# Kernel tuning notes

Hardware: AMD Instinct MI355X
Metric: run time of the kernel (lower is better)

The kernel has to match this reference:

```python
import jax, jax.numpy as jnp
import numpy as np

B, T, D, U = 16, 1600, 512, 1024


def setup_inputs() -> dict:
    key = jax.random.key(0)
    ks = jax.random.split(key, 7)
    sk = 1.0 / np.sqrt(D)
    sr = 1.0 / np.sqrt(U)
    return {
        "x": jax.random.normal(ks[0], (B, T, D), jnp.float32),
        "x_len": jnp.full((B,), T, dtype=jnp.int32),
        "kernel_f": jax.random.normal(ks[1], (D, 4 * U), jnp.float32) * sk,
        "rkernel_f": jax.random.normal(ks[2], (U, 4 * U), jnp.float32) * sr,
        "bias_f": jnp.zeros((4 * U,), jnp.float32),
        "kernel_b": jax.random.normal(ks[3], (D, 4 * U), jnp.float32) * sk,
        "rkernel_b": jax.random.normal(ks[4], (U, 4 * U), jnp.float32) * sr,
        "bias_b": jnp.zeros((4 * U,), jnp.float32),
    }


def _lstm(x, kernel, rkernel, bias):
    """Keras-semantics LSTM, return_sequences=True. x: [B,T,D] -> [B,T,U]."""
    units = rkernel.shape[0]
    # precompute input projection for all timesteps (the big GEMM)
    xg = jnp.einsum('btd,dg->btg', x, kernel) + bias  # [B,T,4U]
    xg = jnp.swapaxes(xg, 0, 1)  # [T,B,4U] for scan
    h0 = jnp.zeros((x.shape[0], units), x.dtype)
    c0 = jnp.zeros((x.shape[0], units), x.dtype)

    def step(carry, g_in):
        h, c = carry
        g = g_in + h @ rkernel  # [B,4U]
        i, f, cc, o = jnp.split(g, 4, axis=-1)  # Keras gate order i,f,c,o
        c = jax.nn.sigmoid(f) * c + jax.nn.sigmoid(i) * jnp.tanh(cc)
        h = jax.nn.sigmoid(o) * jnp.tanh(c)
        return (h, c), h

    _, hs = jax.lax.scan(step, (h0, c0), xg)  # hs: [T,B,U]
    return jnp.swapaxes(hs, 0, 1)


def reference(x, x_len, kernel_f, rkernel_f, bias_f, kernel_b, rkernel_b, bias_b):
    # Bidirectional(LSTM(units, return_sequences=True)), merge_mode='concat'
    out_f = _lstm(x, kernel_f, rkernel_f, bias_f)
    out_b = _lstm(x[:, ::-1], kernel_b, rkernel_b, bias_b)[:, ::-1]
    outputs = jnp.concatenate([out_f, out_b], axis=-1)  # [B,T,2U]
    return outputs, x_len
```

## Files before the change

### kernel.cpp

```cpp
#include <hip/hip_runtime.h>

#define B_   16
#define T_   1600
#define D_   512
#define U_   1024
#define G_   4096
#define NWG  256
#define TPB  256
#define KTOT 1536
#define APAD 1544
#define ROWB (APAD*2)
#define X16OFF (1 << 18)

typedef __attribute__((ext_vector_type(8))) __bf16 bf16x8;
typedef __attribute__((ext_vector_type(4))) float  f32x4;
typedef __attribute__((ext_vector_type(2))) float  f32x2;
typedef __attribute__((ext_vector_type(4))) unsigned int uint4v;
typedef __attribute__((ext_vector_type(8))) unsigned short us8v;
typedef unsigned long long u64;
typedef unsigned int u32;

__device__ __forceinline__ unsigned short f2bf(float f) {
  unsigned u = __builtin_bit_cast(unsigned, f);
  u += 0x7FFFu + ((u >> 16) & 1u);
  return (unsigned short)(u >> 16);
}
__device__ __forceinline__ bf16x8 cvt8(const float4 a, const float4 b) {
  us8v r;
  r[0]=f2bf(a.x); r[1]=f2bf(a.y); r[2]=f2bf(a.z); r[3]=f2bf(a.w);
  r[4]=f2bf(b.x); r[5]=f2bf(b.y); r[6]=f2bf(b.z); r[7]=f2bf(b.w);
  return __builtin_bit_cast(bf16x8, r);
}
__device__ __forceinline__ float sigm(float x){ return 1.f / (1.f + __expf(-x)); }
__device__ __forceinline__ float tanh_(float x){ return 1.f - 2.f / (__expf(2.f*x) + 1.f); }

extern "C" __global__ void __launch_bounds__(256)
xcvt_kernel(const float* __restrict__ xin, unsigned short* __restrict__ x16) {
  const size_t i = ((size_t)blockIdx.x*256 + threadIdx.x) * 8;
  float4 a = *(const float4*)(xin + i);
  float4 b = *(const float4*)(xin + i + 4);
  *(us8v*)(x16 + i) = __builtin_bit_cast(us8v, cvt8(a, b));
}

extern "C" __global__ void __launch_bounds__(TPB, 1)
bilstm_kernel(const float* __restrict__ x, const int* __restrict__ xlen,
              const float* __restrict__ kf, const float* __restrict__ rkf, const float* __restrict__ bf_,
              const float* __restrict__ kb, const float* __restrict__ rkb, const float* __restrict__ bb_,
              float* __restrict__ out, u32* __restrict__ hbuf32,
              const unsigned short* __restrict__ x16, int use16)
{
  extern __shared__ char smem[];

  const int tid = threadIdx.x;
  const int wg  = blockIdx.x;
  const int dir = wg >> 7;
  const int slot = wg & 127;
  const int u0  = slot << 3;

  if (wg == 0 && tid < B_)
    out[(size_t)B_*T_*2*U_ + tid] = (float)xlen[tid];

  const float* Km = dir ? kb  : kf;
  const float* Rm = dir ? rkb : rkf;
  const float* Bv = dir ? bb_ : bf_;

  const int w = tid >> 6, l = tid & 63;
  const int ntile = w & 1, khalf = w >> 1;

  {
    char* Wb = smem;
    for (int i = tid; i < KTOT*32; i += TPB) {
      int k = i >> 5, c = i & 31;
      int gc = ((c >> 3) << 10) + u0 + (c & 7);
      float wv = (k < D_) ? Km[(size_t)k*G_ + gc] : Rm[(size_t)(k-D_)*G_ + gc];
      *(unsigned short*)(Wb + c*ROWB + (k << 1)) = f2bf(wv);
    }
  }
  __syncthreads();

  bf16x8 wx[8], wh[16];
  {
    const char* Brow = smem + (ntile*16 + (l & 15))*ROWB + ((l >> 4) << 4);
    #pragma unroll
    for (int i = 0; i < 8; ++i)  wx[i] = *(const bf16x8*)(Brow + ((khalf*8 + i) << 6));
    #pragma unroll
    for (int i = 0; i < 16; ++i) wh[i] = *(const bf16x8*)(Brow + ((16 + khalf*16 + i) << 6));
  }
  __syncthreads();

  float* gates = (float*)smem;
  char*  hst   = smem + 4096;
  float* gp    = gates + khalf*512;
  const int drow0 = (l >> 4) << 2, dcol = ntile*16 + (l & 15);

  const int eb = tid >> 2, eup = (tid & 3) << 1;
  float bi0=0, bi1=0, bff0=0, bff1=0, bz0=0, bz1=0, bo0=0, bo1=0, c0=0, c1=0;
  if (tid < 64) {
    bi0 = Bv[u0+eup];        bi1 = Bv[u0+eup+1];
    bff0= Bv[1024+u0+eup];   bff1= Bv[1024+u0+eup+1];
    bz0 = Bv[2048+u0+eup];   bz1 = Bv[2048+u0+eup+1];
    bo0 = Bv[3072+u0+eup];   bo1 = Bv[3072+u0+eup+1];
  }

  const float* xbase = x + (size_t)(l & 15)*T_*D_ + khalf*256 + ((l >> 4) << 3);
  const unsigned short* x16b = x16 + (size_t)(l & 15)*T_*D_ + khalf*256 + ((l >> 4) << 3);

  const char* hrow  = hst + (l & 15)*2048;
  const int   kbase = (khalf*512 + ((l >> 4) << 3)) << 1;
  const int   swz   = ((l & 15) & 7) << 4;

  const unsigned off0 = (unsigned)tid * 16;

  f32x4 acc = {0.f, 0.f, 0.f, 0.f};
  {
    const int tg0 = dir ? (T_ - 1) : 0;
    if (use16) {
      const unsigned short* xA = x16b + (size_t)tg0 * D_;
      #pragma unroll
      for (int i = 0; i < 8; ++i)
        acc = __builtin_amdgcn_mfma_f32_16x16x32_bf16(*(const bf16x8*)(xA + i*32), wx[i], acc, 0, 0, 0);
    } else {
      const float* xA = xbase + (size_t)tg0 * D_;
      #pragma unroll
      for (int i = 0; i < 8; ++i) {
        float4 lo = *(const float4*)(xA + i*32);
        float4 hi = *(const float4*)(xA + i*32 + 4);
        acc = __builtin_amdgcn_mfma_f32_16x16x32_bf16(cvt8(lo, hi), wx[i], acc, 0, 0, 0);
      }
    }
  }

  for (int t = 0; t < T_; ++t) {
    const int tg = dir ? (T_ - 1 - t) : t;

    if (t > 0) {
      const u32* hb = hbuf32 + (size_t)((t & 1)*2 + dir) * 16384;
      const unsigned tagv = (unsigned)t << 16;
      uint4v hv[16];
      long long guard = 0;
      for (;;) {
        #pragma unroll
        for (int j = 0; j < 16; ++j)
          asm volatile("global_load_dwordx4 %0, %1, %2 sc0 sc1"
                       : "=v"(hv[j]) : "v"(off0 + (unsigned)(j*4096)), "s"(hb));
        asm volatile("s_waitcnt vmcnt(0)" ::: "memory");
        __builtin_amdgcn_sched_barrier(0);
        unsigned bad = 0;
        #pragma unroll
        for (int j = 0; j < 16; ++j)
          bad |= (hv[j][0] ^ tagv) | (hv[j][2] ^ tagv);
        if (!(bad & 0xFFFF0000u)) break;
        __builtin_amdgcn_s_sleep(1);
        if (++guard > (1LL << 22)) break;
      }
      #pragma unroll
      for (int j = 0; j < 16; ++j) {
        u32 lo = __builtin_amdgcn_perm(hv[j][1], hv[j][0], 0x05040100u);
        u32 hi = __builtin_amdgcn_perm(hv[j][3], hv[j][2], 0x05040100u);
        u64 v = ((u64)hi << 32) | lo;
        *(u64*)(hst + j*2048 + ((tid << 3) ^ ((j & 7) << 4))) = v;
      }
      __syncthreads();

      f32x4 acc2 = {0.f, 0.f, 0.f, 0.f};
      #pragma unroll
      for (int i = 0; i < 16; i += 2) {
        bf16x8 a0 = *(const bf16x8*)(hrow + ((kbase + i*64)     ^ swz));
        bf16x8 a1 = *(const bf16x8*)(hrow + ((kbase + (i+1)*64) ^ swz));
        acc  = __builtin_amdgcn_mfma_f32_16x16x32_bf16(a0, wh[i],   acc,  0, 0, 0);
        acc2 = __builtin_amdgcn_mfma_f32_16x16x32_bf16(a1, wh[i+1], acc2, 0, 0, 0);
      }
      acc[0]+=acc2[0]; acc[1]+=acc2[1]; acc[2]+=acc2[2]; acc[3]+=acc2[3];
    }

    #pragma unroll
    for (int j = 0; j < 4; ++j) gp[(drow0 + j)*32 + dcol] = acc[j];
    __syncthreads();

    if (tid < 64) {
      const float* g0 = gates + eb*32 + eup;
      float gi0 = g0[0]  + g0[512] + bi0,  gi1 = g0[1]  + g0[513] + bi1;
      float gf0 = g0[8]  + g0[520] + bff0, gf1 = g0[9]  + g0[521] + bff1;
      float gz0 = g0[16] + g0[528] + bz0,  gz1 = g0[17] + g0[529] + bz1;
      float go0 = g0[24] + g0[536] + bo0,  go1 = g0[25] + g0[537] + bo1;
      c0 = sigm(gf0)*c0 + sigm(gi0)*tanh_(gz0);
      c1 = sigm(gf1)*c1 + sigm(gi1)*tanh_(gz1);
      float h0 = sigm(go0)*tanh_(c0);
      float h1 = sigm(go1)*tanh_(c1);
      const unsigned tagw = (unsigned)(t + 1) << 16;
      u32 w0 = (u32)f2bf(h0) | tagw;
      u32 w1 = (u32)f2bf(h1) | tagw;
      u32* hdst = hbuf32 + (size_t)(((t & 1) ^ 1)*2 + dir)*16384 + (eb << 10) + u0 + eup;
      __hip_atomic_store((u64*)hdst, ((u64)w1 << 32) | w0, __ATOMIC_RELAXED, __HIP_MEMORY_SCOPE_AGENT);
      f32x2 ho; ho.x = h0; ho.y = h1;
      *(f32x2*)(out + ((size_t)eb*T_ + tg)*(2*U_) + (dir << 10) + u0 + eup) = ho;
    }

    if (t + 1 < T_) {
      const int tg1 = dir ? (T_ - 2 - t) : (t + 1);
      f32x4 nacc = {0.f, 0.f, 0.f, 0.f};
      if (use16) {
        const unsigned short* xA = x16b + (size_t)tg1 * D_;
        #pragma unroll
        for (int i = 0; i < 8; ++i)
          nacc = __builtin_amdgcn_mfma_f32_16x16x32_bf16(*(const bf16x8*)(xA + i*32), wx[i], nacc, 0, 0, 0);
      } else {
        const float* xA = xbase + (size_t)tg1 * D_;
        #pragma unroll
        for (int i = 0; i < 8; ++i) {
          float4 lo = *(const float4*)(xA + i*32);
          float4 hi = *(const float4*)(xA + i*32 + 4);
          nacc = __builtin_amdgcn_mfma_f32_16x16x32_bf16(cvt8(lo, hi), wx[i], nacc, 0, 0, 0);
        }
      }
      acc = nacc;
    }
  }
}

extern "C" void kernel_launch(void* const* d_in, const int* in_sizes, int n_in,
                              void* d_out, int out_size, void* d_ws, size_t ws_size,
                              hipStream_t stream) {
  const float* x   = (const float*)d_in[0];
  const int*   xl  = (const int*)d_in[1];
  const float* kf  = (const float*)d_in[2];
  const float* rkf = (const float*)d_in[3];
  const float* bf_ = (const float*)d_in[4];
  const float* kb  = (const float*)d_in[5];
  const float* rkb = (const float*)d_in[6];
  const float* bb_ = (const float*)d_in[7];
  float* out = (float*)d_out;

  u32* hbuf32 = (u32*)d_ws;
  unsigned short* x16 = (unsigned short*)((char*)d_ws + X16OFF);

  const size_t need = (size_t)X16OFF + (size_t)B_*T_*D_*2;
  const int use16 = (ws_size >= need) ? 1 : 0;

  (void)hipMemsetAsync(d_ws, 0, X16OFF, stream);
  if (use16)
    xcvt_kernel<<<6400, 256, 0, stream>>>(x, x16);

  const size_t smem = 32*(size_t)ROWB;
  bilstm_kernel<<<NWG, TPB, smem, stream>>>(x, xl, kf, rkf, bf_, kb, rkb, bb_,
                                            out, hbuf32, x16, use16);
}
```

Before: 5.185 ms.

## Repartition persistent BiLSTM into 64 large workgroups with LDS-staged x tiles

Shrinks the persistent kernel from 256 workgroups of 256 threads to 64 workgroups of 1024 threads, each owning 32 units (128 gate columns) instead of 8. Fewer workgroups take part in the per-step cross-workgroup spin on the tagged h buffer, and each thread polls 4 loads instead of 16. The x tile is now staged cooperatively into LDS and consumed by MFMA after the barrier, replacing per-wave prefetch from global memory. The trade-off is more work and LDS traffic per workgroup on each serial timestep, and only 64 CUs in use.

```diff
diff --git a/kernel.cpp b/kernel.cpp
--- a/kernel.cpp
+++ b/kernel.cpp
@@ -5,11 +5,14 @@
 #define D_   512
 #define U_   1024
 #define G_   4096
-#define NWG  256
-#define TPB  256
-#define KTOT 1536
-#define APAD 1544
-#define ROWB (APAD*2)
+#define NWG  64
+#define TPB  1024
+#define NCOL 128
+#define GSTR 132
+#define SSTR 392
+#define XBOFF 16896
+#define HOFF  33280
+#define SMEM_BYTES 100352
 #define X16OFF (1 << 18)
 
 typedef __attribute__((ext_vector_type(8))) __bf16 bf16x8;
@@ -51,11 +54,11 @@
 {
   extern __shared__ char smem[];
 
-  const int tid = threadIdx.x;
-  const int wg  = blockIdx.x;
-  const int dir = wg >> 7;
-  const int slot = wg & 127;
-  const int u0  = slot << 3;
+  const int tid  = threadIdx.x;
+  const int wg   = blockIdx.x;
+  const int dir  = wg >> 5;
+  const int slot = wg & 31;
+  const int u0   = slot << 5;
 
   if (wg == 0 && tid < B_)
     out[(size_t)B_*T_*2*U_ + tid] = (float)xlen[tid];
@@ -65,68 +68,76 @@
   const float* Bv = dir ? bb_ : bf_;
 
   const int w = tid >> 6, l = tid & 63;
-  const int ntile = w & 1, khalf = w >> 1;
-
-  {
-    char* Wb = smem;
-    for (int i = tid; i < KTOT*32; i += TPB) {
-      int k = i >> 5, c = i & 31;
-      int gc = ((c >> 3) << 10) + u0 + (c & 7);
-      float wv = (k < D_) ? Km[(size_t)k*G_ + gc] : Rm[(size_t)(k-D_)*G_ + gc];
-      *(unsigned short*)(Wb + c*ROWB + (k << 1)) = f2bf(wv);
-    }
-  }
-  __syncthreads();
+  const int ntile = w >> 1, khalf = w & 1;
+  const int fr8 = (l >> 4) << 3;
+  const int col = ntile*16 + (l & 15);
 
   bf16x8 wx[8], wh[16];
   {
-    const char* Brow = smem + (ntile*16 + (l & 15))*ROWB + ((l >> 4) << 4);
+    unsigned short* stag = (unsigned short*)smem;
     #pragma unroll
-    for (int i = 0; i < 8; ++i)  wx[i] = *(const bf16x8*)(Brow + ((khalf*8 + i) << 6));
+    for (int p = 0; p < 4; ++p) {
+      for (int i = tid; i < 384*NCOL; i += TPB) {
+        int kl = i >> 7, c = i & 127;
+        int k = p*384 + kl;
+        int gc = (c >> 5)*1024 + u0 + (c & 31);
+        float wv = (k < D_) ? Km[(size_t)k*G_ + gc] : Rm[(size_t)(k-D_)*G_ + gc];
+        stag[c*SSTR + kl] = f2bf(wv);
+      }
+      __syncthreads();
+      const unsigned short* srow = stag + col*SSTR;
+      #pragma unroll
+      for (int i = 0; i < 8; ++i) {
+        int kb_ = khalf*256 + i*32;
+        if (kb_/384 == p) wx[i] = *(const bf16x8*)(srow + (kb_ - p*384) + fr8);
+      }
+      #pragma unroll
+      for (int i = 0; i < 16; ++i) {
+        int kb_ = 512 + khalf*512 + i*32;
+        if (kb_/384 == p) wh[i] = *(const bf16x8*)(srow + (kb_ - p*384) + fr8);
+      }
+      __syncthreads();
+    }
+  }
+
+  float* gates = (float*)smem;
+  char*  xbuf  = smem + XBOFF;
+  char*  hst   = smem + HOFF;
+  float* gp    = gates + khalf*(16*GSTR);
+  const int drow0 = (l >> 4) << 2;
+
+  const int eb = tid >> 4, eu = (tid & 15) << 1;
+  float bias[8]; float cc0 = 0.f, cc1 = 0.f;
+  if (tid < 256) {
     #pragma unroll
-    for (int i = 0; i < 16; ++i) wh[i] = *(const bf16x8*)(Brow + ((16 + khalf*16 + i) << 6));
-  }
-  __syncthreads();
-
-  float* gates = (float*)smem;
-  char*  hst   = smem + 4096;
-  float* gp    = gates + khalf*512;
-  const int drow0 = (l >> 4) << 2, dcol = ntile*16 + (l & 15);
-
-  const int eb = tid >> 2, eup = (tid & 3) << 1;
-  float bi0=0, bi1=0, bff0=0, bff1=0, bz0=0, bz1=0, bo0=0, bo1=0, c0=0, c1=0;
-  if (tid < 64) {
-    bi0 = Bv[u0+eup];        bi1 = Bv[u0+eup+1];
-    bff0= Bv[1024+u0+eup];   bff1= Bv[1024+u0+eup+1];
-    bz0 = Bv[2048+u0+eup];   bz1 = Bv[2048+u0+eup+1];
-    bo0 = Bv[3072+u0+eup];   bo1 = Bv[3072+u0+eup+1];
-  }
-
-  const float* xbase = x + (size_t)(l & 15)*T_*D_ + khalf*256 + ((l >> 4) << 3);
-  const unsigned short* x16b = x16 + (size_t)(l & 15)*T_*D_ + khalf*256 + ((l >> 4) << 3);
-
-  const char* hrow  = hst + (l & 15)*2048;
-  const int   kbase = (khalf*512 + ((l >> 4) << 3)) << 1;
-  const int   swz   = ((l & 15) & 7) << 4;
+    for (int g = 0; g < 4; ++g) {
+      bias[g]     = Bv[g*1024 + u0 + eu];
+      bias[4 + g] = Bv[g*1024 + u0 + eu + 1];
+    }
+  }
+
+  const int sxb = tid >> 6, sxk = (tid & 63) << 3;
+  const unsigned short* x16row = x16 + (size_t)sxb*T_*D_ + sxk;
+  const float*          xf32row = x + (size_t)sxb*T_*D_ + sxk;
+  char* xdst = xbuf + sxb*1024;
+  const int xswz = (sxb & 7) << 4;
+
+  const char* xrow = xbuf + (l & 15)*1024;
+  const char* hrow = hst + (l & 15)*2048;
+  const int   swz  = ((l & 15) & 7) << 4;
 
   const unsigned off0 = (unsigned)tid * 16;
-
-  f32x4 acc = {0.f, 0.f, 0.f, 0.f};
+  const int hb_b0 = tid >> 8;
+  const int hb_u  = (tid & 255) << 2;
+
   {
     const int tg0 = dir ? (T_ - 1) : 0;
     if (use16) {
-      const unsigned short* xA = x16b + (size_t)tg0 * D_;
-      #pragma unroll
-      for (int i = 0; i < 8; ++i)
-        acc = __builtin_amdgcn_mfma_f32_16x16x32_bf16(*(const bf16x8*)(xA + i*32), wx[i], acc, 0, 0, 0);
+      *(bf16x8*)(xdst + ((sxk << 1) ^ xswz)) = *(const bf16x8*)(x16row + (size_t)tg0*D_);
     } else {
-      const float* xA = xbase + (size_t)tg0 * D_;
-      #pragma unroll
-      for (int i = 0; i < 8; ++i) {
-        float4 lo = *(const float4*)(xA + i*32);
-        float4 hi = *(const float4*)(xA + i*32 + 4);
-        acc = __builtin_amdgcn_mfma_f32_16x16x32_bf16(cvt8(lo, hi), wx[i], acc, 0, 0, 0);
-      }
+      float4 a = *(const float4*)(xf32row + (size_t)tg0*D_);
+      float4 b = *(const float4*)(xf32row + (size_t)tg0*D_ + 4);
+      *(bf16x8*)(xdst + ((sxk << 1) ^ xswz)) = cvt8(a, b);
     }
   }
 
@@ -136,84 +147,90 @@
     if (t > 0) {
       const u32* hb = hbuf32 + (size_t)((t & 1)*2 + dir) * 16384;
       const unsigned tagv = (unsigned)t << 16;
-      uint4v hv[16];
+      uint4v hv[4];
       long long guard = 0;
       for (;;) {
         #pragma unroll
-        for (int j = 0; j < 16; ++j)
+        for (int j = 0; j < 4; ++j)
           asm volatile("global_load_dwordx4 %0, %1, %2 sc0 sc1"
-                       : "=v"(hv[j]) : "v"(off0 + (unsigned)(j*4096)), "s"(hb));
+                       : "=v"(hv[j]) : "v"(off0 + (unsigned)(j*16384)), "s"(hb));
         asm volatile("s_waitcnt vmcnt(0)" ::: "memory");
         __builtin_amdgcn_sched_barrier(0);
         unsigned bad = 0;
         #pragma unroll
-        for (int j = 0; j < 16; ++j)
+        for (int j = 0; j < 4; ++j)
           bad |= (hv[j][0] ^ tagv) | (hv[j][2] ^ tagv);
         if (!(bad & 0xFFFF0000u)) break;
         __builtin_amdgcn_s_sleep(1);
         if (++guard > (1LL << 22)) break;
       }
       #pragma unroll
-      for (int j = 0; j < 16; ++j) {
+      for (int j = 0; j < 4; ++j) {
         u32 lo = __builtin_amdgcn_perm(hv[j][1], hv[j][0], 0x05040100u);
         u32 hi = __builtin_amdgcn_perm(hv[j][3], hv[j][2], 0x05040100u);
-        u64 v = ((u64)hi << 32) | lo;
-        *(u64*)(hst + j*2048 + ((tid << 3) ^ ((j & 7) << 4))) = v;
-      }
-      __syncthreads();
-
-      f32x4 acc2 = {0.f, 0.f, 0.f, 0.f};
-      #pragma unroll
-      for (int i = 0; i < 16; i += 2) {
-        bf16x8 a0 = *(const bf16x8*)(hrow + ((kbase + i*64)     ^ swz));
-        bf16x8 a1 = *(const bf16x8*)(hrow + ((kbase + (i+1)*64) ^ swz));
-        acc  = __builtin_amdgcn_mfma_f32_16x16x32_bf16(a0, wh[i],   acc,  0, 0, 0);
-        acc2 = __builtin_amdgcn_mfma_f32_16x16x32_bf16(a1, wh[i+1], acc2, 0, 0, 0);
-      }
-      acc[0]+=acc2[0]; acc[1]+=acc2[1]; acc[2]+=acc2[2]; acc[3]+=acc2[3];
-    }
-
-    #pragma unroll
-    for (int j = 0; j < 4; ++j) gp[(drow0 + j)*32 + dcol] = acc[j];
+        const int b = hb_b0 + 4*j;
+        *(u64*)(hst + b*2048 + ((hb_u << 1) ^ ((b & 7) << 4))) = ((u64)hi << 32) | lo;
+      }
+    }
     __syncthreads();
 
-    if (tid < 64) {
-      const float* g0 = gates + eb*32 + eup;
-      float gi0 = g0[0]  + g0[512] + bi0,  gi1 = g0[1]  + g0[513] + bi1;
-      float gf0 = g0[8]  + g0[520] + bff0, gf1 = g0[9]  + g0[521] + bff1;
-      float gz0 = g0[16] + g0[528] + bz0,  gz1 = g0[17] + g0[529] + bz1;
-      float go0 = g0[24] + g0[536] + bo0,  go1 = g0[25] + g0[537] + bo1;
-      c0 = sigm(gf0)*c0 + sigm(gi0)*tanh_(gz0);
-      c1 = sigm(gf1)*c1 + sigm(gi1)*tanh_(gz1);
-      float h0 = sigm(go0)*tanh_(c0);
-      float h1 = sigm(go1)*tanh_(c1);
+    {
+      f32x4 acc = {0.f,0.f,0.f,0.f}, acc2 = acc;
+      #pragma unroll
+      for (int i = 0; i < 8; i += 2) {
+        bf16x8 a0 = *(const bf16x8*)(xrow + (((khalf*8 + i)*64     + (fr8 << 1)) ^ swz));
+        bf16x8 a1 = *(const bf16x8*)(xrow + (((khalf*8 + i + 1)*64 + (fr8 << 1)) ^ swz));
+        acc  = __builtin_amdgcn_mfma_f32_16x16x32_bf16(a0, wx[i],   acc,  0, 0, 0);
+        acc2 = __builtin_amdgcn_mfma_f32_16x16x32_bf16(a1, wx[i+1], acc2, 0, 0, 0);
+      }
+      if (t > 0) {
+        #pragma unroll
+        for (int i = 0; i < 16; i += 2) {
+          bf16x8 a0 = *(const bf16x8*)(hrow + ((khalf*1024 + i*64     + (fr8 << 1)) ^ swz));
+          bf16x8 a1 = *(const bf16x8*)(hrow + ((khalf*1024 + (i+1)*64 + (fr8 << 1)) ^ swz));
+          acc  = __builtin_amdgcn_mfma_f32_16x16x32_bf16(a0, wh[i],   acc,  0, 0, 0);
+          acc2 = __builtin_amdgcn_mfma_f32_16x16x32_bf16(a1, wh[i+1], acc2, 0, 0, 0);
+        }
+      }
+      acc += acc2;
+      #pragma unroll
+      for (int j = 0; j < 4; ++j) gp[(drow0 + j)*GSTR + col] = acc[j];
+    }
+    __syncthreads();
+
+    if (tid < 256) {
+      const float* ga = gates + eb*GSTR + eu;
+      const float* gb2 = gates + (16 + eb)*GSTR + eu;
+      f32x2 ia = *(const f32x2*)(ga);      f32x2 ib = *(const f32x2*)(gb2);
+      f32x2 fa = *(const f32x2*)(ga + 32); f32x2 fb = *(const f32x2*)(gb2 + 32);
+      f32x2 za = *(const f32x2*)(ga + 64); f32x2 zb = *(const f32x2*)(gb2 + 64);
+      f32x2 oa = *(const f32x2*)(ga + 96); f32x2 ob = *(const f32x2*)(gb2 + 96);
+      float gi0 = ia.x + ib.x + bias[0], gi1 = ia.y + ib.y + bias[4];
+      float gf0 = fa.x + fb.x + bias[1], gf1 = fa.y + fb.y + bias[5];
+      float gz0 = za.x + zb.x + bias[2], gz1 = za.y + zb.y + bias[6];
+      float go0 = oa.x + ob.x + bias[3], go1 = oa.y + ob.y + bias[7];
+      cc0 = sigm(gf0)*cc0 + sigm(gi0)*tanh_(gz0);
+      cc1 = sigm(gf1)*cc1 + sigm(gi1)*tanh_(gz1);
+      float h0 = sigm(go0)*tanh_(cc0);
+      float h1 = sigm(go1)*tanh_(cc1);
       const unsigned tagw = (unsigned)(t + 1) << 16;
       u32 w0 = (u32)f2bf(h0) | tagw;
       u32 w1 = (u32)f2bf(h1) | tagw;
-      u32* hdst = hbuf32 + (size_t)(((t & 1) ^ 1)*2 + dir)*16384 + (eb << 10) + u0 + eup;
+      u32* hdst = hbuf32 + (size_t)(((t & 1) ^ 1)*2 + dir)*16384 + (eb << 10) + u0 + eu;
       __hip_atomic_store((u64*)hdst, ((u64)w1 << 32) | w0, __ATOMIC_RELAXED, __HIP_MEMORY_SCOPE_AGENT);
       f32x2 ho; ho.x = h0; ho.y = h1;
-      *(f32x2*)(out + ((size_t)eb*T_ + tg)*(2*U_) + (dir << 10) + u0 + eup) = ho;
+      *(f32x2*)(out + ((size_t)eb*T_ + tg)*(2*U_) + (dir << 10) + u0 + eu) = ho;
     }
 
     if (t + 1 < T_) {
       const int tg1 = dir ? (T_ - 2 - t) : (t + 1);
-      f32x4 nacc = {0.f, 0.f, 0.f, 0.f};
       if (use16) {
-        const unsigned short* xA = x16b + (size_t)tg1 * D_;
-        #pragma unroll
-        for (int i = 0; i < 8; ++i)
-          nacc = __builtin_amdgcn_mfma_f32_16x16x32_bf16(*(const bf16x8*)(xA + i*32), wx[i], nacc, 0, 0, 0);
+        *(bf16x8*)(xdst + ((sxk << 1) ^ xswz)) = *(const bf16x8*)(x16row + (size_t)tg1*D_);
       } else {
-        const float* xA = xbase + (size_t)tg1 * D_;
-        #pragma unroll
-        for (int i = 0; i < 8; ++i) {
-          float4 lo = *(const float4*)(xA + i*32);
-          float4 hi = *(const float4*)(xA + i*32 + 4);
-          nacc = __builtin_amdgcn_mfma_f32_16x16x32_bf16(cvt8(lo, hi), wx[i], nacc, 0, 0, 0);
-        }
-      }
-      acc = nacc;
+        float4 a = *(const float4*)(xf32row + (size_t)tg1*D_);
+        float4 b = *(const float4*)(xf32row + (size_t)tg1*D_ + 4);
+        *(bf16x8*)(xdst + ((sxk << 1) ^ xswz)) = cvt8(a, b);
+      }
     }
   }
 }
@@ -241,7 +258,6 @@
   if (use16)
     xcvt_kernel<<<6400, 256, 0, stream>>>(x, x16);
 
-  const size_t smem = 32*(size_t)ROWB;
-  bilstm_kernel<<<NWG, TPB, smem, stream>>>(x, xl, kf, rkf, bf_, kb, rkb, bb_,
-                                            out, hbuf32, x16, use16);
-}
+  bilstm_kernel<<<NWG, TPB, SMEM_BYTES, stream>>>(x, xl, kf, rkf, bf_, kb, rkb, bb_,
+                                                  out, hbuf32, x16, use16);
+}
```

Result: slower. 11.38 ms (+119.5%).

## Fuse forward and backward LSTM directions into one workgroup per unit slot

Applied to the files above, without the earlier changes.

Halves the grid from 256 to 128 workgroups. Each workgroup now keeps register-resident bf16 weights for both directions and runs a forward section, then a backward section, on every timestep. The aim is to let one direction's recurrent-state polling latency overlap the other direction's compute, and to cut the number of CUs spinning on global flags. In exchange, the per-step critical path inside each workgroup becomes serial across the two directions, half the CUs sit idle, and register pressure roughly doubles.

```diff
diff --git a/kernel.cpp b/kernel.cpp
--- a/kernel.cpp
+++ b/kernel.cpp
@@ -5,7 +5,7 @@
 #define D_   512
 #define U_   1024
 #define G_   4096
-#define NWG  256
+#define NWG  128
 #define TPB  256
 #define KTOT 1536
 #define APAD 1544
@@ -51,42 +51,50 @@
 {
   extern __shared__ char smem[];
 
-  const int tid = threadIdx.x;
-  const int wg  = blockIdx.x;
-  const int dir = wg >> 7;
-  const int slot = wg & 127;
-  const int u0  = slot << 3;
-
-  if (wg == 0 && tid < B_)
+  const int tid  = threadIdx.x;
+  const int slot = blockIdx.x;
+  const int u0   = slot << 3;
+
+  if (slot == 0 && tid < B_)
     out[(size_t)B_*T_*2*U_ + tid] = (float)xlen[tid];
-
-  const float* Km = dir ? kb  : kf;
-  const float* Rm = dir ? rkb : rkf;
-  const float* Bv = dir ? bb_ : bf_;
 
   const int w = tid >> 6, l = tid & 63;
   const int ntile = w & 1, khalf = w >> 1;
 
+  bf16x8 wxf[8], whf[16], wxb[8], whb[16];
   {
     char* Wb = smem;
     for (int i = tid; i < KTOT*32; i += TPB) {
       int k = i >> 5, c = i & 31;
       int gc = ((c >> 3) << 10) + u0 + (c & 7);
-      float wv = (k < D_) ? Km[(size_t)k*G_ + gc] : Rm[(size_t)(k-D_)*G_ + gc];
+      float wv = (k < D_) ? kf[(size_t)k*G_ + gc] : rkf[(size_t)(k-D_)*G_ + gc];
       *(unsigned short*)(Wb + c*ROWB + (k << 1)) = f2bf(wv);
     }
+    __syncthreads();
+    {
+      const char* Brow = smem + (ntile*16 + (l & 15))*ROWB + ((l >> 4) << 4);
+      #pragma unroll
+      for (int i = 0; i < 8; ++i)  wxf[i] = *(const bf16x8*)(Brow + ((khalf*8 + i) << 6));
+      #pragma unroll
+      for (int i = 0; i < 16; ++i) whf[i] = *(const bf16x8*)(Brow + ((16 + khalf*16 + i) << 6));
+    }
+    __syncthreads();
+    for (int i = tid; i < KTOT*32; i += TPB) {
+      int k = i >> 5, c = i & 31;
+      int gc = ((c >> 3) << 10) + u0 + (c & 7);
+      float wv = (k < D_) ? kb[(size_t)k*G_ + gc] : rkb[(size_t)(k-D_)*G_ + gc];
+      *(unsigned short*)(Wb + c*ROWB + (k << 1)) = f2bf(wv);
+    }
+    __syncthreads();
+    {
+      const char* Brow = smem + (ntile*16 + (l & 15))*ROWB + ((l >> 4) << 4);
+      #pragma unroll
+      for (int i = 0; i < 8; ++i)  wxb[i] = *(const bf16x8*)(Brow + ((khalf*8 + i) << 6));
+      #pragma unroll
+      for (int i = 0; i < 16; ++i) whb[i] = *(const bf16x8*)(Brow + ((16 + khalf*16 + i) << 6));
+    }
+    __syncthreads();
   }
-  __syncthreads();
-
-  bf16x8 wx[8], wh[16];
-  {
-    const char* Brow = smem + (ntile*16 + (l & 15))*ROWB + ((l >> 4) << 4);
-    #pragma unroll
-    for (int i = 0; i < 8; ++i)  wx[i] = *(const bf16x8*)(Brow + ((khalf*8 + i) << 6));
-    #pragma unroll
-    for (int i = 0; i < 16; ++i) wh[i] = *(const bf16x8*)(Brow + ((16 + khalf*16 + i) << 6));
-  }
-  __syncthreads();
 
   float* gates = (float*)smem;
   char*  hst   = smem + 4096;
@@ -94,12 +102,16 @@
   const int drow0 = (l >> 4) << 2, dcol = ntile*16 + (l & 15);
 
   const int eb = tid >> 2, eup = (tid & 3) << 1;
-  float bi0=0, bi1=0, bff0=0, bff1=0, bz0=0, bz1=0, bo0=0, bo1=0, c0=0, c1=0;
+  float bfr[8] = {0,0,0,0,0,0,0,0}, bbr[8] = {0,0,0,0,0,0,0,0};
+  float cf0=0, cf1=0, cb0=0, cb1=0;
   if (tid < 64) {
-    bi0 = Bv[u0+eup];        bi1 = Bv[u0+eup+1];
-    bff0= Bv[1024+u0+eup];   bff1= Bv[1024+u0+eup+1];
-    bz0 = Bv[2048+u0+eup];   bz1 = Bv[2048+u0+eup+1];
-    bo0 = Bv[3072+u0+eup];   bo1 = Bv[3072+u0+eup+1];
+    #pragma unroll
+    for (int g = 0; g < 4; ++g) {
+      bfr[2*g]   = bf_[(g << 10) + u0 + eup];
+      bfr[2*g+1] = bf_[(g << 10) + u0 + eup + 1];
+      bbr[2*g]   = bb_[(g << 10) + u0 + eup];
+      bbr[2*g+1] = bb_[(g << 10) + u0 + eup + 1];
+    }
   }
 
   const float* xbase = x + (size_t)(l & 15)*T_*D_ + khalf*256 + ((l >> 4) << 3);
@@ -108,113 +120,105 @@
   const char* hrow  = hst + (l & 15)*2048;
   const int   kbase = (khalf*512 + ((l >> 4) << 3)) << 1;
   const int   swz   = ((l & 15) & 7) << 4;
-
   const unsigned off0 = (unsigned)tid * 16;
 
-  f32x4 acc = {0.f, 0.f, 0.f, 0.f};
-  {
-    const int tg0 = dir ? (T_ - 1) : 0;
-    if (use16) {
-      const unsigned short* xA = x16b + (size_t)tg0 * D_;
-      #pragma unroll
-      for (int i = 0; i < 8; ++i)
-        acc = __builtin_amdgcn_mfma_f32_16x16x32_bf16(*(const bf16x8*)(xA + i*32), wx[i], acc, 0, 0, 0);
-    } else {
-      const float* xA = xbase + (size_t)tg0 * D_;
-      #pragma unroll
-      for (int i = 0; i < 8; ++i) {
-        float4 lo = *(const float4*)(xA + i*32);
-        float4 hi = *(const float4*)(xA + i*32 + 4);
-        acc = __builtin_amdgcn_mfma_f32_16x16x32_bf16(cvt8(lo, hi), wx[i], acc, 0, 0, 0);
-      }
-    }
-  }
+#define XPROJ(nacc, wxA, tgi)                                                            \
+  do {                                                                                   \
+    if (use16) {                                                                         \
+      const unsigned short* xA = x16b + (size_t)(tgi) * D_;                              \
+      _Pragma("unroll")                                                                  \
+      for (int i = 0; i < 8; ++i)                                                        \
+        nacc = __builtin_amdgcn_mfma_f32_16x16x32_bf16(*(const bf16x8*)(xA + i*32),      \
+                                                       wxA[i], nacc, 0, 0, 0);           \
+    } else {                                                                             \
+      const float* xA = xbase + (size_t)(tgi) * D_;                                      \
+      _Pragma("unroll")                                                                  \
+      for (int i = 0; i < 8; ++i) {                                                      \
+        float4 lo = *(const float4*)(xA + i*32);                                         \
+        float4 hi = *(const float4*)(xA + i*32 + 4);                                     \
+        nacc = __builtin_amdgcn_mfma_f32_16x16x32_bf16(cvt8(lo, hi), wxA[i], nacc,       \
+                                                       0, 0, 0);                         \
+      }                                                                                  \
+    }                                                                                    \
+  } while (0)
+
+  f32x4 accf = {0.f,0.f,0.f,0.f}, accb = {0.f,0.f,0.f,0.f};
+  XPROJ(accf, wxf, 0);
+  XPROJ(accb, wxb, T_ - 1);
+
+#define SECTION(DIR, acc, whA, wxA, biasA, cc0, cc1, tg_cur, tg_next)                    \
+  do {                                                                                   \
+    if (t > 0) {                                                                         \
+      const u32* hb = hbuf32 + (size_t)((t & 1)*2 + DIR) * 16384;                        \
+      const unsigned tagv = (unsigned)t << 16;                                           \
+      uint4v hv[16];                                                                     \
+      long long guard = 0;                                                               \
+      for (;;) {                                                                         \
+        _Pragma("unroll")                                                                \
+        for (int j = 0; j < 16; ++j)                                                     \
+          asm volatile("global_load_dwordx4 %0, %1, %2 sc0 sc1"                          \
+                       : "=v"(hv[j]) : "v"(off0 + (unsigned)(j*4096)), "s"(hb));         \
+        asm volatile("s_waitcnt vmcnt(0)" ::: "memory");                                 \
+        __builtin_amdgcn_sched_barrier(0);                                               \
+        unsigned bad = 0;                                                                \
+        _Pragma("unroll")                                                                \
+        for (int j = 0; j < 16; ++j)                                                     \
+          bad |= (hv[j][0] ^ tagv) | (hv[j][2] ^ tagv);                                  \
+        if (!(bad & 0xFFFF0000u)) break;                                                 \
+        __builtin_amdgcn_s_sleep(1);                                                     \
+        if (++guard > (1LL << 22)) break;                                                \
+      }                                                                                  \
+      _Pragma("unroll")                                                                  \
+      for (int j = 0; j < 16; ++j) {                                                     \
+        u32 lo = __builtin_amdgcn_perm(hv[j][1], hv[j][0], 0x05040100u);                 \
+        u32 hi = __builtin_amdgcn_perm(hv[j][3], hv[j][2], 0x05040100u);                 \
+        *(u64*)(hst + j*2048 + ((tid << 3) ^ ((j & 7) << 4))) = ((u64)hi << 32) | lo;    \
+      }                                                                                  \
+    }                                                                                    \
+    __syncthreads();                \
+    if (t > 0) {                                                                         \
+      f32x4 a2 = {0.f,0.f,0.f,0.f};                                                      \
+      _Pragma("unroll")                                                                  \
+      for (int i = 0; i < 16; i += 2) {                                                  \
+        bf16x8 a0 = *(const bf16x8*)(hrow + ((kbase + i*64)     ^ swz));                 \
+        bf16x8 a1 = *(const bf16x8*)(hrow + ((kbase + (i+1)*64) ^ swz));                 \
+        acc = __builtin_amdgcn_mfma_f32_16x16x32_bf16(a0, whA[i],   acc, 0, 0, 0);       \
+        a2  = __builtin_amdgcn_mfma_f32_16x16x32_bf16(a1, whA[i+1], a2,  0, 0, 0);       \
+      }                                                                                  \
+      acc[0]+=a2[0]; acc[1]+=a2[1]; acc[2]+=a2[2]; acc[3]+=a2[3];                        \
+    }                                                                                    \
+    _Pragma("unroll")                                                                    \
+    for (int j = 0; j < 4; ++j) gp[(drow0 + j)*32 + dcol] = acc[j];                      \
+    __syncthreads();                                \
+    if (tid < 64) {                                                                      \
+      const float* g0 = gates + eb*32 + eup;                                             \
+      float gi0 = g0[0]  + g0[512] + biasA[0], gi1 = g0[1]  + g0[513] + biasA[1];        \
+      float gf0 = g0[8]  + g0[520] + biasA[2], gf1 = g0[9]  + g0[521] + biasA[3];        \
+      float gz0 = g0[16] + g0[528] + biasA[4], gz1 = g0[17] + g0[529] + biasA[5];        \
+      float go0 = g0[24] + g0[536] + biasA[6], go1 = g0[25] + g0[537] + biasA[7];        \
+      cc0 = sigm(gf0)*cc0 + sigm(gi0)*tanh_(gz0);                                        \
+      cc1 = sigm(gf1)*cc1 + sigm(gi1)*tanh_(gz1);                                        \
+      float h0 = sigm(go0)*tanh_(cc0);                                                   \
+      float h1 = sigm(go1)*tanh_(cc1);                                                   \
+      const unsigned tagw = (unsigned)(t + 1) << 16;                                     \
+      u32 w0 = (u32)f2bf(h0) | tagw;                                                     \
+      u32 w1 = (u32)f2bf(h1) | tagw;                                                     \
+      u32* hdst = hbuf32 + (size_t)(((t & 1) ^ 1)*2 + DIR)*16384 + (eb << 10) + u0 + eup;\
+      __hip_atomic_store((u64*)hdst, ((u64)w1 << 32) | w0, __ATOMIC_RELAXED,             \
+                         __HIP_MEMORY_SCOPE_AGENT);                                      \
+      f32x2 ho; ho.x = h0; ho.y = h1;                                                    \
+      *(f32x2*)(out + ((size_t)eb*T_ + (tg_cur))*(2*U_) + (DIR << 10) + u0 + eup) = ho;  \
+    }                                                                                    \
+    if (t + 1 < T_) {                                                                    \
+      f32x4 nacc = {0.f,0.f,0.f,0.f};                                                    \
+      XPROJ(nacc, wxA, tg_next);                                                         \
+      acc = nacc;                                                                        \
+    }                                                                                    \
+  } while (0)
 
   for (int t = 0; t < T_; ++t) {
-    const int tg = dir ? (T_ - 1 - t) : t;
-
-    if (t > 0) {
-      const u32* hb = hbuf32 + (size_t)((t & 1)*2 + dir) * 16384;
-      const unsigned tagv = (unsigned)t << 16;
-      uint4v hv[16];
-      long long guard = 0;
-      for (;;) {
-        #pragma unroll
-        for (int j = 0; j < 16; ++j)
-          asm volatile("global_load_dwordx4 %0, %1, %2 sc0 sc1"
-                       : "=v"(hv[j]) : "v"(off0 + (unsigned)(j*4096)), "s"(hb));
-        asm volatile("s_waitcnt vmcnt(0)" ::: "memory");
-        __builtin_amdgcn_sched_barrier(0);
-        unsigned bad = 0;
-        #pragma unroll
-        for (int j = 0; j < 16; ++j)
-          bad |= (hv[j][0] ^ tagv) | (hv[j][2] ^ tagv);
-        if (!(bad & 0xFFFF0000u)) break;
-        __builtin_amdgcn_s_sleep(1);
-        if (++guard > (1LL << 22)) break;
-      }
-      #pragma unroll
-      for (int j = 0; j < 16; ++j) {
-        u32 lo = __builtin_amdgcn_perm(hv[j][1], hv[j][0], 0x05040100u);
-        u32 hi = __builtin_amdgcn_perm(hv[j][3], hv[j][2], 0x05040100u);
-        u64 v = ((u64)hi << 32) | lo;
-        *(u64*)(hst + j*2048 + ((tid << 3) ^ ((j & 7) << 4))) = v;
-      }
-      __syncthreads();
-
-      f32x4 acc2 = {0.f, 0.f, 0.f, 0.f};
-      #pragma unroll
-      for (int i = 0; i < 16; i += 2) {
-        bf16x8 a0 = *(const bf16x8*)(hrow + ((kbase + i*64)     ^ swz));
-        bf16x8 a1 = *(const bf16x8*)(hrow + ((kbase + (i+1)*64) ^ swz));
-        acc  = __builtin_amdgcn_mfma_f32_16x16x32_bf16(a0, wh[i],   acc,  0, 0, 0);
-        acc2 = __builtin_amdgcn_mfma_f32_16x16x32_bf16(a1, wh[i+1], acc2, 0, 0, 0);
-      }
-      acc[0]+=acc2[0]; acc[1]+=acc2[1]; acc[2]+=acc2[2]; acc[3]+=acc2[3];
-    }
-
-    #pragma unroll
-    for (int j = 0; j < 4; ++j) gp[(drow0 + j)*32 + dcol] = acc[j];
-    __syncthreads();
-
-    if (tid < 64) {
-      const float* g0 = gates + eb*32 + eup;
-      float gi0 = g0[0]  + g0[512] + bi0,  gi1 = g0[1]  + g0[513] + bi1;
-      float gf0 = g0[8]  + g0[520] + bff0, gf1 = g0[9]  + g0[521] + bff1;
-      float gz0 = g0[16] + g0[528] + bz0,  gz1 = g0[17] + g0[529] + bz1;
-      float go0 = g0[24] + g0[536] + bo0,  go1 = g0[25] + g0[537] + bo1;
-      c0 = sigm(gf0)*c0 + sigm(gi0)*tanh_(gz0);
-      c1 = sigm(gf1)*c1 + sigm(gi1)*tanh_(gz1);
-      float h0 = sigm(go0)*tanh_(c0);
-      float h1 = sigm(go1)*tanh_(c1);
-      const unsigned tagw = (unsigned)(t + 1) << 16;
-      u32 w0 = (u32)f2bf(h0) | tagw;
-      u32 w1 = (u32)f2bf(h1) | tagw;
-      u32* hdst = hbuf32 + (size_t)(((t & 1) ^ 1)*2 + dir)*16384 + (eb << 10) + u0 + eup;
-      __hip_atomic_store((u64*)hdst, ((u64)w1 << 32) | w0, __ATOMIC_RELAXED, __HIP_MEMORY_SCOPE_AGENT);
-      f32x2 ho; ho.x = h0; ho.y = h1;
-      *(f32x2*)(out + ((size_t)eb*T_ + tg)*(2*U_) + (dir << 10) + u0 + eup) = ho;
-    }
-
-    if (t + 1 < T_) {
-      const int tg1 = dir ? (T_ - 2 - t) : (t + 1);
-      f32x4 nacc = {0.f, 0.f, 0.f, 0.f};
-      if (use16) {
-        const unsigned short* xA = x16b + (size_t)tg1 * D_;
-        #pragma unroll
-        for (int i = 0; i < 8; ++i)
-          nacc = __builtin_amdgcn_mfma_f32_16x16x32_bf16(*(const bf16x8*)(xA + i*32), wx[i], nacc, 0, 0, 0);
-      } else {
-        const float* xA = xbase + (size_t)tg1 * D_;
-        #pragma unroll
-        for (int i = 0; i < 8; ++i) {
-          float4 lo = *(const float4*)(xA + i*32);
-          float4 hi = *(const float4*)(xA + i*32 + 4);
-          nacc = __builtin_amdgcn_mfma_f32_16x16x32_bf16(cvt8(lo, hi), wx[i], nacc, 0, 0, 0);
-        }
-      }
-      acc = nacc;
-    }
+    SECTION(0, accf, whf, wxf, bfr, cf0, cf1, t,          t + 1);
+    SECTION(1, accb, whb, wxb, bbr, cb0, cb1, T_ - 1 - t, T_ - 2 - t);
   }
 }
 
```

Result: slower. 12.08 ms (+133.0%).
